# Optimization experiments

Hardware: AMD Instinct MI355X
Metric: run time of the kernel (lower is better)

Reference implementation:

```python
import jax, jax.numpy as jnp
import numpy as np

N_NODES = 100000
N_EDGES = 1600000


def gcn_conv(x, src, dst, W, b, n_nodes):
    # PyG GCNConv: h = x @ W; symmetric normalization with self-loops; scatter-add; + bias
    deg = jax.ops.segment_sum(jnp.ones_like(src, dtype=x.dtype), dst, num_segments=n_nodes)
    dinv = jax.lax.rsqrt(jnp.where(deg > 0, deg, 1.0))
    norm = dinv[src] * dinv[dst]              # [E+N]
    h = x @ W                                  # [N, out]
    msg = h[src] * norm[:, None]               # gather + scale (irregular access)
    out = jax.ops.segment_sum(msg, dst, num_segments=n_nodes)  # scatter-add aggregate
    return out + b


def setup_inputs() -> dict:
    key = jax.random.key(0)
    k1, k2, k3, k4 = jax.random.split(key, 4)
    x = jax.random.normal(k1, (N_NODES, 128), dtype=jnp.float32)
    edge_index = jax.random.randint(k2, (2, N_EDGES), 0, N_NODES, dtype=jnp.int64)
    W1 = jax.random.normal(k3, (128, 48), dtype=jnp.float32) * (1.0 / np.sqrt(128))
    b1 = jnp.zeros((48,), dtype=jnp.float32)
    W2 = jax.random.normal(k4, (48, 16), dtype=jnp.float32) * (1.0 / np.sqrt(48))
    b2 = jnp.zeros((16,), dtype=jnp.float32)
    return {"x": x, "edge_index": edge_index, "W1": W1, "b1": b1, "W2": W2, "b2": b2}


def reference(x, edge_index, W1, b1, W2, b2):
    n = x.shape[0]
    loops = jnp.arange(n, dtype=edge_index.dtype)
    src = jnp.concatenate([edge_index[0], loops])  # add self-loops
    dst = jnp.concatenate([edge_index[1], loops])
    h = gcn_conv(x, src, dst, W1, b1, n)
    h = jax.nn.relu(h)
    h = gcn_conv(h, src, dst, W2, b2, n)
    h = jax.nn.relu(h)
    return jax.nn.softmax(h, axis=1)
```

## Files before the change

kernel.cpp:

```cpp
#include <hip/hip_runtime.h>
#include <hip/hip_bf16.h>
#include <hip/hip_fp16.h>


#define TILE 8192

typedef _Float16 half8 __attribute__((ext_vector_type(8)));
typedef float floatx4 __attribute__((ext_vector_type(4)));

__global__ __launch_bounds__(256) void k_bhist(const int* __restrict__ dst, int E,
                                               int* __restrict__ Hw, int nbuck) {
    __shared__ int h[512];
    int t = threadIdx.x;
    for (int i = t; i < nbuck; i += 256) h[i] = 0;
    __syncthreads();
    int base = blockIdx.x * TILE;
#pragma unroll
    for (int r = 0; r < TILE / 256; ++r) {
        int e = base + r * 256 + t;
        if (e < E) atomicAdd(&h[dst[e] >> 8], 1);
    }
    __syncthreads();
    for (int i = t; i < nbuck; i += 256) Hw[blockIdx.x * nbuck + i] = h[i];
}

__global__ __launch_bounds__(256) void k_bsum(const int* __restrict__ Hw, int nTiles,
                                              int nbuck, int* __restrict__ btot) {
    int wid = (blockIdx.x * 256 + threadIdx.x) >> 6;
    int lane = threadIdx.x & 63;
    if (wid >= nbuck) return;
    int sum = 0;
    for (int tt = lane; tt < nTiles; tt += 64) sum += Hw[tt * nbuck + wid];
#pragma unroll
    for (int off = 32; off; off >>= 1) sum += __shfl_down(sum, off);
    if (lane == 0) btot[wid] = sum;
}

__global__ __launch_bounds__(512) void k_bscan2(const int* __restrict__ btot, int nbuck,
                                                int* __restrict__ bstart) {
    __shared__ int s[512];
    int t = threadIdx.x;
    int v = (t < nbuck) ? btot[t] : 0;
    s[t] = v;
    __syncthreads();
    for (int off = 1; off < 512; off <<= 1) {
        int tmp = (t >= off) ? s[t - off] : 0;
        __syncthreads();
        s[t] += tmp;
        __syncthreads();
    }
    if (t < nbuck) bstart[t] = s[t] - v;
    if (t == nbuck - 1) bstart[nbuck] = s[t];
}

__global__ __launch_bounds__(256) void k_boff(int* __restrict__ Hw, int nTiles,
                                              int nbuck, const int* __restrict__ bstart) {
    int wid = (blockIdx.x * 256 + threadIdx.x) >> 6;
    int lane = threadIdx.x & 63;
    if (wid >= nbuck) return;
    int running = bstart[wid];
    for (int chunk = 0; chunk < nTiles; chunk += 64) {
        int tt = chunk + lane;
        int v = (tt < nTiles) ? Hw[tt * nbuck + wid] : 0;
        int incl = v;
#pragma unroll
        for (int off = 1; off < 64; off <<= 1) {
            int u = __shfl_up(incl, off);
            if (lane >= off) incl += u;
        }
        if (tt < nTiles) Hw[tt * nbuck + wid] = running + (incl - v);
        running += __shfl(incl, 63);
    }
}

__global__ __launch_bounds__(256) void k_bscatter(const int* __restrict__ ei, int E,
                                                  const int* __restrict__ Hw, int nbuck,
                                                  int* __restrict__ ebuf) {
    __shared__ int cur[512];
    int t = threadIdx.x;
    for (int i = t; i < nbuck; i += 256) cur[i] = Hw[blockIdx.x * nbuck + i];
    __syncthreads();
    int base = blockIdx.x * TILE;
#pragma unroll
    for (int r = 0; r < TILE / 256; ++r) {
        int e = base + r * 256 + t;
        if (e < E) {
            int s = ei[e];
            int d = ei[E + e];
            int pos = atomicAdd(&cur[d >> 8], 1);
            ebuf[pos] = s | ((d & 255) << 17);
        }
    }
}

__global__ __launch_bounds__(256) void k_csrfill(const int* __restrict__ ebuf,
                                                 const int* __restrict__ bstart,
                                                 int* __restrict__ csr,
                                                 int* __restrict__ rowstart,
                                                 int* __restrict__ deg,
                                                 float* __restrict__ dinv, int N) {
    __shared__ int lcnt[256];
    __shared__ int lscan[256];
    __shared__ int lcur[256];
    int t = threadIdx.x;
    int nodebase = blockIdx.x << 8;
    int segs = bstart[blockIdx.x];
    int sege = bstart[blockIdx.x + 1];
    lcnt[t] = 0;
    __syncthreads();
    for (int i = segs + t; i < sege; i += 256)
        atomicAdd(&lcnt[((unsigned)ebuf[i]) >> 17], 1);
    __syncthreads();
    int v = lcnt[t];
    lscan[t] = v;
    __syncthreads();
    for (int off = 1; off < 256; off <<= 1) {
        int tmp = (t >= off) ? lscan[t - off] : 0;
        __syncthreads();
        lscan[t] += tmp;
        __syncthreads();
    }
    int excl = lscan[t] - v;
    int node = nodebase + t;
    if (node < N) {
        rowstart[node] = segs + excl;
        deg[node] = v;
        dinv[node] = rsqrtf((float)(v + 1));
    }
    lcur[t] = segs + excl;
    __syncthreads();
    for (int i = segs + t; i < sege; i += 256) {
        int pk = ebuf[i];
        int pos = atomicAdd(&lcur[((unsigned)pk) >> 17], 1);
        csr[pos] = pk & 0x1FFFF;
    }
}

__global__ __launch_bounds__(256) void k_gemm1(const float* __restrict__ x,
                                               const float* __restrict__ W1,
                                               const float* __restrict__ dinv,
                                               __half* __restrict__ h1p, int N) {
    __shared__ _Float16 wt[48 * 136];
    int t = threadIdx.x;
    for (int i = t; i < 128 * 48; i += 256) {
        int k = i / 48, c = i % 48;
        wt[c * 136 + k] = (_Float16)W1[i];
    }
    __syncthreads();

    int wave = t >> 6, lane = t & 63;
    int g = lane >> 4;
    int rtile = blockIdx.x * 64 + wave * 16;
    int rowA = rtile + (lane & 15);
    const float* xrow = x + (size_t)(rowA < N ? rowA : N - 1) * 128;
    int c0 = lane & 15;

    floatx4 acc[3];
#pragma unroll
    for (int nt = 0; nt < 3; ++nt)
#pragma unroll
        for (int q = 0; q < 4; ++q) acc[nt][q] = 0.f;

#pragma unroll
    for (int kc = 0; kc < 4; ++kc) {
        int k0 = kc * 32 + g * 8;
        float4 a0 = *(const float4*)(xrow + k0);
        float4 a1 = *(const float4*)(xrow + k0 + 4);
        half8 a;
        a[0] = (_Float16)a0.x; a[1] = (_Float16)a0.y;
        a[2] = (_Float16)a0.z; a[3] = (_Float16)a0.w;
        a[4] = (_Float16)a1.x; a[5] = (_Float16)a1.y;
        a[6] = (_Float16)a1.z; a[7] = (_Float16)a1.w;
#pragma unroll
        for (int nt = 0; nt < 3; ++nt) {
            half8 b = *(const half8*)(&wt[(nt * 16 + c0) * 136 + k0]);
            acc[nt] = __builtin_amdgcn_mfma_f32_16x16x32_f16(a, b, acc[nt], 0, 0, 0);
        }
    }

    int rbase = rtile + g * 4;
#pragma unroll
    for (int j = 0; j < 4; ++j) {
        int r = rbase + j;
        if (r < N) {
            float dr = dinv[r];
#pragma unroll
            for (int nt = 0; nt < 3; ++nt)
                h1p[(size_t)r * 48 + nt * 16 + c0] = __float2half(acc[nt][j] * dr);
        }
    }
}

__global__ __launch_bounds__(256) void k_agg1(const __half* __restrict__ h1p,
                                              const int* __restrict__ csr,
                                              const int* __restrict__ rowstart,
                                              const int* __restrict__ deg,
                                              const float* __restrict__ dinv,
                                              const float* __restrict__ b1,
                                              float* __restrict__ r1, int N) {
    int wave = threadIdx.x >> 6;
    int lane = threadIdx.x & 63;
    int v = blockIdx.x * 4 + wave;
    if (v >= N) return;
    int grp = lane >> 3;
    int sub = lane & 7;

    int start = rowstart[v];
    int d = deg[v];
    float dv = dinv[v];
    const int* cs = csr + start;
    const char* h1b = (const char*)h1p;

    float acc[8] = {0.f, 0.f, 0.f, 0.f, 0.f, 0.f, 0.f, 0.f};

    for (int base = 0; base < d; base += 64) {
        int sreg = (base + lane < d) ? cs[base + lane] : 0;
        int nb = min(64, d - base);
        for (int j = 0; j < 8 && j * 8 < nb; ++j) {
            int s = __shfl(sreg, j * 8 + grp);
            if (j * 8 + grp < nb && sub < 6) {
                float4 rv = *(const float4*)(h1b + (size_t)s * 96 + sub * 16);
                const __half2* hp = (const __half2*)&rv;
#pragma unroll
                for (int q = 0; q < 4; ++q) {
                    float2 f = __half22float2(hp[q]);
                    acc[q * 2] += f.x;
                    acc[q * 2 + 1] += f.y;
                }
            }
        }
    }
#pragma unroll
    for (int i = 0; i < 8; ++i) {
        acc[i] += __shfl_xor(acc[i], 8);
        acc[i] += __shfl_xor(acc[i], 16);
        acc[i] += __shfl_xor(acc[i], 32);
    }
    if (grp == 0 && sub < 6) {
        float4 sv = *(const float4*)(h1b + (size_t)v * 96 + sub * 16);
        const __half2* hp = (const __half2*)&sv;
        float o[8];
#pragma unroll
        for (int q = 0; q < 4; ++q) {
            float2 f = __half22float2(hp[q]);
            o[q * 2]     = fmaxf(dv * (acc[q * 2] + f.x) + b1[sub * 8 + q * 2], 0.f);
            o[q * 2 + 1] = fmaxf(dv * (acc[q * 2 + 1] + f.y) + b1[sub * 8 + q * 2 + 1], 0.f);
        }
        float4* dst = (float4*)(r1 + (size_t)v * 48 + sub * 8);
        dst[0] = make_float4(o[0], o[1], o[2], o[3]);
        dst[1] = make_float4(o[4], o[5], o[6], o[7]);
    }
}

__global__ __launch_bounds__(256) void k_gemm2(const float* __restrict__ r1,
                                               const float* __restrict__ W2,
                                               const float* __restrict__ dinv,
                                               __half* __restrict__ h2p, int N) {
    __shared__ float w2s[48 * 16];
    int t = threadIdx.x;
    for (int i = t; i < 768; i += 256) w2s[i] = W2[i];
    __syncthreads();
    int flat = blockIdx.x * 256 + t;
    int row = flat >> 2;
    int cg = (flat & 3) * 4;
    if (row >= N) return;
    float4 acc = make_float4(0.f, 0.f, 0.f, 0.f);
    const float* xr = r1 + (size_t)row * 48;
    for (int kk = 0; kk < 48; kk += 4) {
        float4 a = *(const float4*)(xr + kk);
#pragma unroll
        for (int j = 0; j < 4; j++) {
            float av = (j == 0) ? a.x : (j == 1) ? a.y : (j == 2) ? a.z : a.w;
            float4 b = *(const float4*)(w2s + (kk + j) * 16 + cg);
            acc.x += av * b.x;
            acc.y += av * b.y;
            acc.z += av * b.z;
            acc.w += av * b.w;
        }
    }
    float dr = dinv[row];
    __half2 h01 = __floats2half2_rn(acc.x * dr, acc.y * dr);
    __half2 h23 = __floats2half2_rn(acc.z * dr, acc.w * dr);
    __half* dst = h2p + (size_t)row * 16 + cg;
    *(__half2*)(dst) = h01;
    *(__half2*)(dst + 2) = h23;
}

__global__ __launch_bounds__(256) void k_agg2(const __half* __restrict__ h2p,
                                              const int* __restrict__ csr,
                                              const int* __restrict__ rowstart,
                                              const int* __restrict__ deg,
                                              const float* __restrict__ dinv,
                                              const float* __restrict__ b2,
                                              float* __restrict__ out, int N) {
    int tid = threadIdx.x;
    int lane = tid & 63;
    int hf = lane >> 5;
    int l32 = lane & 31;
    int grp = l32 >> 1;
    int sub = lane & 1;
    int v = (blockIdx.x * 4 + (tid >> 6)) * 2 + hf;
    if (v >= N) return;

    int start = rowstart[v];
    int d = deg[v];
    float dv = dinv[v];
    const int* cs = csr + start;
    const char* h2b = (const char*)h2p;

    float acc[8] = {0.f, 0.f, 0.f, 0.f, 0.f, 0.f, 0.f, 0.f};

    for (int base = 0; base < d; base += 32) {
        int sreg = (base + l32 < d) ? cs[base + l32] : 0;
        int nb = min(32, d - base);
        for (int j = 0; j < 2 && j * 16 < nb; ++j) {
            int s = __shfl(sreg, (hf << 5) + j * 16 + grp);
            if (j * 16 + grp < nb) {
                float4 rv = *(const float4*)(h2b + (size_t)s * 32 + sub * 16);
                const __half2* hp = (const __half2*)&rv;
#pragma unroll
                for (int q = 0; q < 4; ++q) {
                    float2 f = __half22float2(hp[q]);
                    acc[q * 2] += f.x;
                    acc[q * 2 + 1] += f.y;
                }
            }
        }
    }
#pragma unroll
    for (int i = 0; i < 8; ++i) {
        acc[i] += __shfl_xor(acc[i], 2);
        acc[i] += __shfl_xor(acc[i], 4);
        acc[i] += __shfl_xor(acc[i], 8);
        acc[i] += __shfl_xor(acc[i], 16);
    }
    if (grp == 0) {
        float4 sv = *(const float4*)(h2b + (size_t)v * 32 + sub * 16);
        const __half2* hp = (const __half2*)&sv;
        float z[8];
#pragma unroll
        for (int q = 0; q < 4; ++q) {
            float2 f = __half22float2(hp[q]);
            z[q * 2]     = fmaxf(dv * (acc[q * 2] + f.x) + b2[sub * 8 + q * 2], 0.f);
            z[q * 2 + 1] = fmaxf(dv * (acc[q * 2 + 1] + f.y) + b2[sub * 8 + q * 2 + 1], 0.f);
        }
        float m8 = z[0];
#pragma unroll
        for (int i = 1; i < 8; ++i) m8 = fmaxf(m8, z[i]);
        float m = fmaxf(m8, __shfl_xor(m8, 1));
        float p[8];
        float s8 = 0.f;
#pragma unroll
        for (int i = 0; i < 8; ++i) { p[i] = __expf(z[i] - m); s8 += p[i]; }
        float inv = 1.f / (s8 + __shfl_xor(s8, 1));
        float4* dst = (float4*)(out + (size_t)v * 16 + sub * 8);
        dst[0] = make_float4(p[0] * inv, p[1] * inv, p[2] * inv, p[3] * inv);
        dst[1] = make_float4(p[4] * inv, p[5] * inv, p[6] * inv, p[7] * inv);
    }
}

extern "C" void kernel_launch(void* const* d_in, const int* in_sizes, int n_in,
                              void* d_out, int out_size, void* d_ws, size_t ws_size,
                              hipStream_t stream) {
    const float* x  = (const float*)d_in[0];
    const int*   ei = (const int*)d_in[1];
    const float* W1 = (const float*)d_in[2];
    const float* b1 = (const float*)d_in[3];
    const float* W2 = (const float*)d_in[4];
    const float* b2 = (const float*)d_in[5];
    float* out = (float*)d_out;

    int N = in_sizes[0] / 128;
    int E = in_sizes[1] / 2;
    int NBK = (N + 255) >> 8;
    int nTiles = (E + TILE - 1) / TILE;

    char* p = (char*)d_ws;
    auto alloc = [&](size_t bytes) -> char* {
        char* q = p;
        p += (bytes + 255) & ~(size_t)255;
        return q;
    };
    int*    deg      = (int*)alloc((size_t)N * 4);
    int*    rowstart = (int*)alloc((size_t)N * 4);
    float*  dinv     = (float*)alloc((size_t)N * 4);
    int*    btot     = (int*)alloc((size_t)NBK * 4);
    int*    bstart   = (int*)alloc((size_t)(NBK + 1) * 4);
    int*    Hw       = (int*)alloc((size_t)nTiles * NBK * 4);
    int*    csr      = (int*)alloc((size_t)E * 4);
    size_t  ovl_sz   = (size_t)N * 48 * 2 > (size_t)E * 4 ? (size_t)N * 48 * 2
                                                          : (size_t)E * 4;
    char*   ovl      = alloc(ovl_sz);
    int*    ebuf     = (int*)ovl;
    __half* h1p      = (__half*)ovl;
    float*  r1       = (float*)alloc((size_t)N * 48 * 4);
    __half* h2p      = h1p;

    int wgBuck = (NBK + 3) / 4;

    hipLaunchKernelGGL(k_bhist, dim3(nTiles), dim3(256), 0, stream, ei + E, E, Hw, NBK);
    hipLaunchKernelGGL(k_bsum, dim3(wgBuck), dim3(256), 0, stream, Hw, nTiles, NBK, btot);
    hipLaunchKernelGGL(k_bscan2, dim3(1), dim3(512), 0, stream, btot, NBK, bstart);
    hipLaunchKernelGGL(k_boff, dim3(wgBuck), dim3(256), 0, stream, Hw, nTiles, NBK, bstart);
    hipLaunchKernelGGL(k_bscatter, dim3(nTiles), dim3(256), 0, stream, ei, E, Hw, NBK, ebuf);
    hipLaunchKernelGGL(k_csrfill, dim3(NBK), dim3(256), 0, stream,
                       ebuf, bstart, csr, rowstart, deg, dinv, N);
    hipLaunchKernelGGL(k_gemm1, dim3((N + 63) / 64), dim3(256), 0, stream,
                       x, W1, dinv, h1p, N);
    hipLaunchKernelGGL(k_agg1, dim3((N + 3) / 4), dim3(256), 0, stream,
                       h1p, csr, rowstart, deg, dinv, b1, r1, N);
    hipLaunchKernelGGL(k_gemm2, dim3((N * 4 + 255) / 256), dim3(256), 0, stream,
                       r1, W2, dinv, h2p, N);
    hipLaunchKernelGGL(k_agg2, dim3((N + 7) / 8), dim3(256), 0, stream,
                       h2p, csr, rowstart, deg, dinv, b2, out, N);
}
```

Before: 148.0 us.

## Split layer-1 aggregation into column chunks and store ReLU output as fp16

Layer-1 aggregation now launches three grid slices, each covering a 32-byte column chunk of the 96-byte fp16 rows. Each wave can then handle 32 edges per gather step with every lane active, instead of 8 edges with 2 of 8 lanes idle. The intermediate r1 is stored as fp16, halving its write and its read in gemm2, and gemm2 is rewritten to consume half2 pairs. The cost is that the CSR index list and degree metadata are read three times, one per chunk, and r1 loses precision. The agg2 inner loop is also unrolled with fixed trip counts.

```diff
diff --git a/kernel.cpp b/kernel.cpp
--- a/kernel.cpp
+++ b/kernel.cpp
@@ -191,35 +191,42 @@
     }
 }
 
-__global__ __launch_bounds__(256) void k_agg1(const __half* __restrict__ h1p,
-                                              const int* __restrict__ csr,
-                                              const int* __restrict__ rowstart,
-                                              const int* __restrict__ deg,
-                                              const float* __restrict__ dinv,
-                                              const float* __restrict__ b1,
-                                              float* __restrict__ r1, int N) {
+__global__ __launch_bounds__(256) void k_agg1c(const __half* __restrict__ h1p,
+                                               const int* __restrict__ csr,
+                                               const int* __restrict__ rowstart,
+                                               const int* __restrict__ deg,
+                                               const float* __restrict__ dinv,
+                                               const float* __restrict__ b1,
+                                               __half* __restrict__ r1h, int N,
+                                               int nblk) {
+    int bid = blockIdx.x;
+    int c = bid / nblk;
+    int vb = bid % nblk;
     int wave = threadIdx.x >> 6;
     int lane = threadIdx.x & 63;
-    int v = blockIdx.x * 4 + wave;
+    int v = vb * 4 + wave;
     if (v >= N) return;
-    int grp = lane >> 3;
-    int sub = lane & 7;
+    int grp = lane >> 1;
+    int sub = lane & 1;
 
     int start = rowstart[v];
     int d = deg[v];
     float dv = dinv[v];
     const int* cs = csr + start;
     const char* h1b = (const char*)h1p;
+    int coff = c * 32 + sub * 16;
 
     float acc[8] = {0.f, 0.f, 0.f, 0.f, 0.f, 0.f, 0.f, 0.f};
 
     for (int base = 0; base < d; base += 64) {
+        int nb = min(64, d - base);
         int sreg = (base + lane < d) ? cs[base + lane] : 0;
-        int nb = min(64, d - base);
-        for (int j = 0; j < 8 && j * 8 < nb; ++j) {
-            int s = __shfl(sreg, j * 8 + grp);
-            if (j * 8 + grp < nb && sub < 6) {
-                float4 rv = *(const float4*)(h1b + (size_t)s * 96 + sub * 16);
+#pragma unroll
+        for (int j = 0; j < 2; ++j) {
+            int e = j * 32 + grp;
+            int s = __shfl(sreg, e);
+            if (e < nb) {
+                float4 rv = *(const float4*)(h1b + (size_t)s * 96 + coff);
                 const __half2* hp = (const __half2*)&rv;
 #pragma unroll
                 for (int q = 0; q < 4; ++q) {
@@ -232,27 +239,29 @@
     }
 #pragma unroll
     for (int i = 0; i < 8; ++i) {
+        acc[i] += __shfl_xor(acc[i], 2);
+        acc[i] += __shfl_xor(acc[i], 4);
         acc[i] += __shfl_xor(acc[i], 8);
         acc[i] += __shfl_xor(acc[i], 16);
         acc[i] += __shfl_xor(acc[i], 32);
     }
-    if (grp == 0 && sub < 6) {
-        float4 sv = *(const float4*)(h1b + (size_t)v * 96 + sub * 16);
+    if (grp == 0) {
+        float4 sv = *(const float4*)(h1b + (size_t)v * 96 + coff);
         const __half2* hp = (const __half2*)&sv;
-        float o[8];
+        __half2 ob[4];
 #pragma unroll
         for (int q = 0; q < 4; ++q) {
-            float2 f = __half22float2(hp[q]);
-            o[q * 2]     = fmaxf(dv * (acc[q * 2] + f.x) + b1[sub * 8 + q * 2], 0.f);
-            o[q * 2 + 1] = fmaxf(dv * (acc[q * 2 + 1] + f.y) + b1[sub * 8 + q * 2 + 1], 0.f);
-        }
-        float4* dst = (float4*)(r1 + (size_t)v * 48 + sub * 8);
-        dst[0] = make_float4(o[0], o[1], o[2], o[3]);
-        dst[1] = make_float4(o[4], o[5], o[6], o[7]);
-    }
-}
-
-__global__ __launch_bounds__(256) void k_gemm2(const float* __restrict__ r1,
+            float2 sf = __half22float2(hp[q]);
+            int fi = c * 16 + sub * 8 + q * 2;
+            float o0 = fmaxf(dv * (acc[q * 2] + sf.x) + b1[fi], 0.f);
+            float o1 = fmaxf(dv * (acc[q * 2 + 1] + sf.y) + b1[fi + 1], 0.f);
+            ob[q] = __floats2half2_rn(o0, o1);
+        }
+        *(float4*)((char*)r1h + (size_t)v * 96 + coff) = *(const float4*)ob;
+    }
+}
+
+__global__ __launch_bounds__(256) void k_gemm2(const __half* __restrict__ r1h,
                                                const float* __restrict__ W2,
                                                const float* __restrict__ dinv,
                                                __half* __restrict__ h2p, int N) {
@@ -265,18 +274,16 @@
     int cg = (flat & 3) * 4;
     if (row >= N) return;
     float4 acc = make_float4(0.f, 0.f, 0.f, 0.f);
-    const float* xr = r1 + (size_t)row * 48;
-    for (int kk = 0; kk < 48; kk += 4) {
-        float4 a = *(const float4*)(xr + kk);
-#pragma unroll
-        for (int j = 0; j < 4; j++) {
-            float av = (j == 0) ? a.x : (j == 1) ? a.y : (j == 2) ? a.z : a.w;
-            float4 b = *(const float4*)(w2s + (kk + j) * 16 + cg);
-            acc.x += av * b.x;
-            acc.y += av * b.y;
-            acc.z += av * b.z;
-            acc.w += av * b.w;
-        }
+    const __half2* xr = (const __half2*)((const char*)r1h + (size_t)row * 96);
+#pragma unroll 4
+    for (int kk = 0; kk < 24; ++kk) {
+        float2 a = __half22float2(xr[kk]);
+        float4 b0 = *(const float4*)(w2s + (2 * kk) * 16 + cg);
+        float4 b1v = *(const float4*)(w2s + (2 * kk + 1) * 16 + cg);
+        acc.x += a.x * b0.x + a.y * b1v.x;
+        acc.y += a.x * b0.y + a.y * b1v.y;
+        acc.z += a.x * b0.z + a.y * b1v.z;
+        acc.w += a.x * b0.w + a.y * b1v.w;
     }
     float dr = dinv[row];
     __half2 h01 = __floats2half2_rn(acc.x * dr, acc.y * dr);
@@ -313,9 +320,11 @@
     for (int base = 0; base < d; base += 32) {
         int sreg = (base + l32 < d) ? cs[base + l32] : 0;
         int nb = min(32, d - base);
-        for (int j = 0; j < 2 && j * 16 < nb; ++j) {
-            int s = __shfl(sreg, (hf << 5) + j * 16 + grp);
-            if (j * 16 + grp < nb) {
+#pragma unroll
+        for (int j = 0; j < 2; ++j) {
+            int e = j * 16 + grp;
+            int s = __shfl(sreg, (hf << 5) + e);
+            if (e < nb) {
                 float4 rv = *(const float4*)(h2b + (size_t)s * 32 + sub * 16);
                 const __half2* hp = (const __half2*)&rv;
 #pragma unroll
@@ -393,10 +402,11 @@
     char*   ovl      = alloc(ovl_sz);
     int*    ebuf     = (int*)ovl;
     __half* h1p      = (__half*)ovl;
-    float*  r1       = (float*)alloc((size_t)N * 48 * 4);
+    __half* r1h      = (__half*)alloc((size_t)N * 48 * 2);
     __half* h2p      = h1p;
 
     int wgBuck = (NBK + 3) / 4;
+    int nblkAgg = (N + 3) / 4;
 
     hipLaunchKernelGGL(k_bhist, dim3(nTiles), dim3(256), 0, stream, ei + E, E, Hw, NBK);
     hipLaunchKernelGGL(k_bsum, dim3(wgBuck), dim3(256), 0, stream, Hw, nTiles, NBK, btot);
@@ -407,10 +417,10 @@
                        ebuf, bstart, csr, rowstart, deg, dinv, N);
     hipLaunchKernelGGL(k_gemm1, dim3((N + 63) / 64), dim3(256), 0, stream,
                        x, W1, dinv, h1p, N);
-    hipLaunchKernelGGL(k_agg1, dim3((N + 3) / 4), dim3(256), 0, stream,
-                       h1p, csr, rowstart, deg, dinv, b1, r1, N);
+    hipLaunchKernelGGL(k_agg1c, dim3(3 * nblkAgg), dim3(256), 0, stream,
+                       h1p, csr, rowstart, deg, dinv, b1, r1h, N, nblkAgg);
     hipLaunchKernelGGL(k_gemm2, dim3((N * 4 + 255) / 256), dim3(256), 0, stream,
-                       r1, W2, dinv, h2p, N);
+                       r1h, W2, dinv, h2p, N);
     hipLaunchKernelGGL(k_agg2, dim3((N + 7) / 8), dim3(256), 0, stream,
                        h2p, csr, rowstart, deg, dinv, b2, out, N);
 }
```

Measured after the change: 231.6 us. +56.5%, slower.
